# Optimization experiments

Measured on AMD Instinct MI355X. Metric: run time of the kernel, lower is better.

Reference implementation:

```python
import jax, jax.numpy as jnp
import numpy as np

B, N, C, L = 32, 1024, 128, 4

def setup_inputs() -> dict:
    key = jax.random.key(0)
    ks = jax.random.split(key, 8)
    x = jax.random.normal(ks[0], (B, N, C), dtype=jnp.float32)
    # binary adjacency: nonzero entries become unit-weight edges (edge weights unused in module)
    adj = jax.random.randint(ks[1], (B, N, N), 0, 2).astype(jnp.float32)
    mask = jnp.ones((B, N), dtype=jnp.float32)
    s = 1.0 / np.sqrt(C)
    weight = jax.random.uniform(ks[2], (L, C, C), minval=-s, maxval=s, dtype=jnp.float32)
    w_ih = jax.random.uniform(ks[3], (L, 3 * C, C), minval=-s, maxval=s, dtype=jnp.float32)
    w_hh = jax.random.uniform(ks[4], (L, 3 * C, C), minval=-s, maxval=s, dtype=jnp.float32)
    b_ih = jax.random.uniform(ks[5], (L, 3 * C), minval=-s, maxval=s, dtype=jnp.float32)
    b_hh = jax.random.uniform(ks[6], (L, 3 * C), minval=-s, maxval=s, dtype=jnp.float32)
    return {"x": x, "adj": adj, "mask": mask, "weight": weight,
            "w_ih": w_ih, "w_hh": w_hh, "b_ih": b_ih, "b_hh": b_hh}

def _gru_cell(m, h, w_ih, w_hh, b_ih, b_hh):
    # PyTorch GRUCell, gate order (r, z, n)
    gx = m @ w_ih.T + b_ih
    gh = h @ w_hh.T + b_hh
    xr, xz, xn = jnp.split(gx, 3, axis=-1)
    hr, hz, hn = jnp.split(gh, 3, axis=-1)
    r = jax.nn.sigmoid(xr + hr)
    z = jax.nn.sigmoid(xz + hz)
    n = jnp.tanh(xn + r * hn)
    return (1.0 - z) * n + z * h

def reference(x, adj, mask, weight, w_ih, w_hh, b_ih, b_hh):
    h = x  # [B, N, C]; in_channels == out_channels so no zero-padding needed
    for i in range(L):
        hw = jnp.einsum('bnc,cd->bnd', h, weight[i])
        # scatter-add of messages source->target == A^T @ (h W), unit edge weights
        m = jnp.einsum('bjn,bjd->bnd', adj, hw)
        h = _gru_cell(m, h, w_ih[i], w_hh[i], b_ih[i], b_hh[i])
    return h * mask[:, :, None]
```

## Files before the change

### kernel.cpp

```cpp
#include <hip/hip_runtime.h>
#include <stdint.h>


#define NB 32
#define NN 1024
#define NC 128
#define NL 4
#define MTOT (NB * NN)

#define KT 64
#define PITCH 72

typedef __attribute__((ext_vector_type(8))) short s16x8;
typedef __attribute__((ext_vector_type(4))) float f32x4;
typedef __attribute__((ext_vector_type(2))) unsigned int u32x2;
typedef unsigned short U16;
typedef unsigned int U32;

__device__ __forceinline__ U16 f2bf(float f) {
    union { float f; U32 u; } v; v.f = f;
    return (U16)((v.u + 0x7FFFu + ((v.u >> 16) & 1u)) >> 16);
}
__device__ __forceinline__ float bf2f(U16 h) {
    union { U32 u; float f; } v; v.u = ((U32)h) << 16;
    return v.f;
}
__device__ __forceinline__ void splitbf(float x, U16& hi, U16& lo) {
    hi = f2bf(x);
    lo = f2bf(x - bf2f(hi));
}
__device__ __forceinline__ float sigmoidf_(float x) { return 1.f / (1.f + __expf(-x)); }

__device__ __forceinline__ void glds16(const void* g, void* l) {
    __builtin_amdgcn_global_load_lds(
        (const __attribute__((address_space(1))) void*)g,
        (__attribute__((address_space(3))) void*)l, 16, 0, 0);
}

__global__ __launch_bounds__(256) void k_setup(
    const float* __restrict__ adj, U16* __restrict__ adjT,
    const float* __restrict__ w, const float* __restrict__ wih, const float* __restrict__ whh,
    U16* __restrict__ wThi, U16* __restrict__ wTlo,
    U16* __restrict__ wihhi, U16* __restrict__ wihlo,
    U16* __restrict__ whhhi, U16* __restrict__ whhlo,
    const float* __restrict__ x, U16* __restrict__ hhi, U16* __restrict__ hlo)
{
    __shared__ float t[64 * 65];
    const int bid = blockIdx.x, tid = threadIdx.x;
    if (bid < 8192) {
        const int b = bid >> 8, rem = bid & 255;
        const int j0 = (rem & 15) * 64, n0 = (rem >> 4) * 64;
        const int rr = tid >> 4, c4 = (tid & 15) * 4;
#pragma unroll
        for (int p = 0; p < 4; ++p) {
            int j = p * 16 + rr;
            f32x4 v = *(const f32x4*)&adj[((size_t)b << 20) + ((size_t)(j0 + j) << 10) + n0 + c4];
#pragma unroll
            for (int u = 0; u < 4; ++u) t[j * 65 + c4 + u] = v[u];
        }
        __syncthreads();
#pragma unroll
        for (int p = 0; p < 4; ++p) {
            int n = p * 16 + rr;
            U16 h0 = f2bf(t[(c4 + 0) * 65 + n]);
            U16 h1 = f2bf(t[(c4 + 1) * 65 + n]);
            U16 h2 = f2bf(t[(c4 + 2) * 65 + n]);
            U16 h3 = f2bf(t[(c4 + 3) * 65 + n]);
            u32x2 pk; pk[0] = (U32)h0 | ((U32)h1 << 16); pk[1] = (U32)h2 | ((U32)h3 << 16);
            *(u32x2*)&adjT[((size_t)b << 20) + ((size_t)(n0 + n) << 10) + j0 + c4] = pk;
        }
    } else if (bid < 9984) {
        int i = (bid - 8192) * 256 + tid;
        if (i < 65536) {
            int l = i >> 14, rem = i & 16383, c = rem >> 7, d = rem & 127;
            U16 hi, lo; splitbf(w[i], hi, lo);
            int o = (l << 14) + (d << 7) + c;
            wThi[o] = hi; wTlo[o] = lo;
        } else if (i < 262144) {
            int j = i - 65536;
            U16 hi, lo; splitbf(wih[j], hi, lo);
            wihhi[j] = hi; wihlo[j] = lo;
        } else {
            int j = i - 262144;
            U16 hi, lo; splitbf(whh[j], hi, lo);
            whhhi[j] = hi; whhlo[j] = lo;
        }
    } else {
        int base = (bid - 9984) * 2048 + tid;
#pragma unroll
        for (int p = 0; p < 8; ++p) {
            int i = base + p * 256;
            U16 hi, lo; splitbf(x[i], hi, lo);
            hhi[i] = hi; hlo[i] = lo;
        }
    }
}

struct __align__(16) Smem3 {
    union {
        struct { U16 A[2][128 * PITCH]; U16 B[2][128 * PITCH]; } s;
        float bounce[128 * 129];
    };
};

__global__ __launch_bounds__(256, 2) void k_hw(
    const U16* __restrict__ Ahi, const U16* __restrict__ Alo,
    const U16* __restrict__ Bhi, const U16* __restrict__ Blo,
    U16* __restrict__ Ohi, U16* __restrict__ Olo)
{
    __shared__ Smem3 sm;
    const int tid = threadIdx.x;
    const int lane = tid & 63, wv = tid >> 6;
    const int wr = (wv & 1) * 64, wc = (wv >> 1) * 64;
    const int lm = lane & 15, lk8 = (lane >> 4) * 8;
    const int m0 = blockIdx.x * 128;

    f32x4 acc[4][4] = {};

    for (int kc = 0; kc < 128; kc += KT) {
#pragma unroll
        for (int t = 0; t < 4; ++t) {
            int i = tid + t * 256; int r = i >> 3, v = (i & 7) * 8;
            *(s16x8*)&sm.s.A[0][r * PITCH + v] = *(const s16x8*)&Ahi[(size_t)(m0 + r) * 128 + kc + v];
            *(s16x8*)&sm.s.A[1][r * PITCH + v] = *(const s16x8*)&Alo[(size_t)(m0 + r) * 128 + kc + v];
        }
#pragma unroll
        for (int t = 0; t < 4; ++t) {
            int i = tid + t * 256; int r = i >> 3, v = (i & 7) * 8;
            *(s16x8*)&sm.s.B[0][r * PITCH + v] = *(const s16x8*)&Bhi[r * 128 + kc + v];
            *(s16x8*)&sm.s.B[1][r * PITCH + v] = *(const s16x8*)&Blo[r * 128 + kc + v];
        }
        __syncthreads();
#pragma unroll
        for (int ks = 0; ks < 2; ++ks) {
            const int ko = ks * 32 + lk8;
            s16x8 ahi[4], alo[4], bhi[4], blo[4];
#pragma unroll
            for (int q = 0; q < 4; ++q) {
                ahi[q] = *(const s16x8*)&sm.s.A[0][(wr + q * 16 + lm) * PITCH + ko];
                alo[q] = *(const s16x8*)&sm.s.A[1][(wr + q * 16 + lm) * PITCH + ko];
                bhi[q] = *(const s16x8*)&sm.s.B[0][(wc + q * 16 + lm) * PITCH + ko];
                blo[q] = *(const s16x8*)&sm.s.B[1][(wc + q * 16 + lm) * PITCH + ko];
            }
#pragma unroll
            for (int rt = 0; rt < 4; ++rt)
#pragma unroll
                for (int ct = 0; ct < 4; ++ct) {
                    f32x4 a = acc[rt][ct];
                    a = __builtin_amdgcn_mfma_f32_16x16x32_bf16(ahi[rt], bhi[ct], a, 0, 0, 0);
                    a = __builtin_amdgcn_mfma_f32_16x16x32_bf16(ahi[rt], blo[ct], a, 0, 0, 0);
                    a = __builtin_amdgcn_mfma_f32_16x16x32_bf16(alo[rt], bhi[ct], a, 0, 0, 0);
                    acc[rt][ct] = a;
                }
        }
        __syncthreads();
    }
#pragma unroll
    for (int rt = 0; rt < 4; ++rt)
#pragma unroll
        for (int ct = 0; ct < 4; ++ct)
#pragma unroll
            for (int r = 0; r < 4; ++r)
                sm.bounce[(wr + rt * 16 + (lane >> 4) * 4 + r) * 129 + wc + ct * 16 + lm] = acc[rt][ct][r];
    __syncthreads();
    const int b = m0 >> 10, j0 = m0 & 1023;
    for (int t = 0; t < 32; ++t) {
        int i = tid + t * 256; int d = i >> 6, j2 = (i & 63) * 2;
        float x0 = sm.bounce[j2 * 129 + d], x1 = sm.bounce[(j2 + 1) * 129 + d];
        U16 h0, l0, h1, l1; splitbf(x0, h0, l0); splitbf(x1, h1, l1);
        size_t o = (((size_t)(b * 128 + d)) << 10) + j0 + j2;
        *(U32*)&Ohi[o] = (U32)h0 | ((U32)h1 << 16);
        *(U32*)&Olo[o] = (U32)l0 | ((U32)l1 << 16);
    }
}

__global__ __launch_bounds__(256, 2) void k_mega2(
    const U16* __restrict__ adjT,
    const U16* __restrict__ hwThi, const U16* __restrict__ hwTlo,
    U16* mhi, U16* mlo,
    const U16* __restrict__ hhi, const U16* __restrict__ hlo,
    const U16* __restrict__ wihhi, const U16* __restrict__ wihlo,
    const U16* __restrict__ whhhi, const U16* __restrict__ whhlo,
    const float* __restrict__ bih, const float* __restrict__ bhh,
    const float* __restrict__ mask,
    U16* __restrict__ houthi, U16* __restrict__ houtlo,
    float* __restrict__ out, int last)
{
    __shared__ U16 As[64 * 64];
    __shared__ U16 Bh[128 * 64];
    __shared__ U16 Bl[128 * 64];
    const int tid = threadIdx.x;
    const int lane = tid & 63, wv = tid >> 6;
    const int wd0 = wv * 32;
    const int lm = lane & 15, lk8 = (lane >> 4) * 8, quad = lane >> 4;
    const int bt = blockIdx.x >> 4;
    const int n0 = (blockIdx.x & 15) * 64;
    const int row0 = bt * NN + n0;

    f32x4 macc[4][2] = {};
    for (int kc = 0; kc < NN; kc += 64) {
#pragma unroll
        for (int t = 0; t < 2; ++t) {
            int li = tid + t * 256; int r = li >> 3, sg = li & 7;
            glds16(&adjT[((size_t)bt << 20) + ((size_t)(n0 + r) << 10) + kc + sg * 8],
                   &As[li * 8]);
        }
#pragma unroll
        for (int t = 0; t < 4; ++t) {
            int li = tid + t * 256; int d = li >> 3, sg = li & 7;
            size_t o = (((size_t)(bt * 128 + d)) << 10) + kc + sg * 8;
            glds16(&hwThi[o], &Bh[li * 8]);
            glds16(&hwTlo[o], &Bl[li * 8]);
        }
        __syncthreads();
#pragma unroll
        for (int ks = 0; ks < 2; ++ks) {
            const int ko = ks * 32 + lk8;
            s16x8 a[4], bh[2], bl[2];
#pragma unroll
            for (int q = 0; q < 4; ++q)
                a[q] = *(const s16x8*)&As[(q * 16 + lm) * 64 + ko];
#pragma unroll
            for (int q = 0; q < 2; ++q) {
                bh[q] = *(const s16x8*)&Bh[(wd0 + q * 16 + lm) * 64 + ko];
                bl[q] = *(const s16x8*)&Bl[(wd0 + q * 16 + lm) * 64 + ko];
            }
#pragma unroll
            for (int rt = 0; rt < 4; ++rt)
#pragma unroll
                for (int ct = 0; ct < 2; ++ct) {
                    f32x4 c = macc[rt][ct];
                    c = __builtin_amdgcn_mfma_f32_16x16x32_bf16(a[rt], bh[ct], c, 0, 0, 0);
                    c = __builtin_amdgcn_mfma_f32_16x16x32_bf16(a[rt], bl[ct], c, 0, 0, 0);
                    macc[rt][ct] = c;
                }
        }
        __syncthreads();
    }

#pragma unroll
    for (int rt = 0; rt < 4; ++rt)
#pragma unroll
        for (int ct = 0; ct < 2; ++ct)
#pragma unroll
            for (int rr = 0; rr < 4; ++rr) {
                int rloc = rt * 16 + quad * 4 + rr;
                int d = wd0 + ct * 16 + lm;
                U16 hi, lo; splitbf(macc[rt][ct][rr], hi, lo);
                size_t o = (size_t)(row0 + rloc) * 128 + d;
                mhi[o] = hi; mlo[o] = lo;
            }
    __syncthreads();

    f32x4 aR[4][2], aZ[4][2], aXN[4][2], aHN[4][2];
#pragma unroll
    for (int ct = 0; ct < 2; ++ct) {
        const int col = wd0 + ct * 16 + lm;
        const float bR  = bih[col]       + bhh[col];
        const float bZ  = bih[128 + col] + bhh[128 + col];
        const float bXN = bih[256 + col];
        const float bHN = bhh[256 + col];
#pragma unroll
        for (int rt = 0; rt < 4; ++rt) {
            aR[rt][ct]  = f32x4{bR, bR, bR, bR};
            aZ[rt][ct]  = f32x4{bZ, bZ, bZ, bZ};
            aXN[rt][ct] = f32x4{bXN, bXN, bXN, bXN};
            aHN[rt][ct] = f32x4{bHN, bHN, bHN, bHN};
        }
    }

    for (int ch = 0; ch < 4; ++ch) {
        const U16* Ahi = (ch < 2) ? (const U16*)mhi : hhi;
        const U16* Alo = (ch < 2) ? (const U16*)mlo : hlo;
        const U16* __restrict__ Whi = (ch < 2) ? wihhi : whhhi;
        const U16* __restrict__ Wlo = (ch < 2) ? wihlo : whhlo;
        const int kb = (ch & 1) * 64;
#pragma unroll
        for (int ks = 0; ks < 2; ++ks) {
            const int ko = kb + ks * 32 + lk8;
            s16x8 ahi[4], alo[4];
#pragma unroll
            for (int q = 0; q < 4; ++q) {
                size_t ao = (size_t)(row0 + q * 16 + lm) * 128 + ko;
                ahi[q] = *(const s16x8*)&Ahi[ao];
                alo[q] = *(const s16x8*)&Alo[ao];
            }
#pragma unroll
            for (int ct = 0; ct < 2; ++ct) {
                const int col = wd0 + ct * 16 + lm;
                s16x8 bhiR = *(const s16x8*)&Whi[(size_t)col * 128 + ko];
                s16x8 bloR = *(const s16x8*)&Wlo[(size_t)col * 128 + ko];
                s16x8 bhiZ = *(const s16x8*)&Whi[(size_t)(128 + col) * 128 + ko];
                s16x8 bloZ = *(const s16x8*)&Wlo[(size_t)(128 + col) * 128 + ko];
                s16x8 bhiN = *(const s16x8*)&Whi[(size_t)(256 + col) * 128 + ko];
                s16x8 bloN = *(const s16x8*)&Wlo[(size_t)(256 + col) * 128 + ko];
#pragma unroll
                for (int rt = 0; rt < 4; ++rt) {
                    f32x4 r = aR[rt][ct];
                    r = __builtin_amdgcn_mfma_f32_16x16x32_bf16(ahi[rt], bhiR, r, 0, 0, 0);
                    r = __builtin_amdgcn_mfma_f32_16x16x32_bf16(ahi[rt], bloR, r, 0, 0, 0);
                    r = __builtin_amdgcn_mfma_f32_16x16x32_bf16(alo[rt], bhiR, r, 0, 0, 0);
                    aR[rt][ct] = r;
                    f32x4 z = aZ[rt][ct];
                    z = __builtin_amdgcn_mfma_f32_16x16x32_bf16(ahi[rt], bhiZ, z, 0, 0, 0);
                    z = __builtin_amdgcn_mfma_f32_16x16x32_bf16(ahi[rt], bloZ, z, 0, 0, 0);
                    z = __builtin_amdgcn_mfma_f32_16x16x32_bf16(alo[rt], bhiZ, z, 0, 0, 0);
                    aZ[rt][ct] = z;
                }
                if (ch < 2) {
#pragma unroll
                    for (int rt = 0; rt < 4; ++rt) {
                        f32x4 n = aXN[rt][ct];
                        n = __builtin_amdgcn_mfma_f32_16x16x32_bf16(ahi[rt], bhiN, n, 0, 0, 0);
                        n = __builtin_amdgcn_mfma_f32_16x16x32_bf16(ahi[rt], bloN, n, 0, 0, 0);
                        n = __builtin_amdgcn_mfma_f32_16x16x32_bf16(alo[rt], bhiN, n, 0, 0, 0);
                        aXN[rt][ct] = n;
                    }
                } else {
#pragma unroll
                    for (int rt = 0; rt < 4; ++rt) {
                        f32x4 n = aHN[rt][ct];
                        n = __builtin_amdgcn_mfma_f32_16x16x32_bf16(ahi[rt], bhiN, n, 0, 0, 0);
                        n = __builtin_amdgcn_mfma_f32_16x16x32_bf16(ahi[rt], bloN, n, 0, 0, 0);
                        n = __builtin_amdgcn_mfma_f32_16x16x32_bf16(alo[rt], bhiN, n, 0, 0, 0);
                        aHN[rt][ct] = n;
                    }
                }
            }
        }
    }

#pragma unroll
    for (int rt = 0; rt < 4; ++rt) {
#pragma unroll
        for (int ct = 0; ct < 2; ++ct) {
            const int col = wd0 + ct * 16 + lm;
#pragma unroll
            for (int rr = 0; rr < 4; ++rr) {
                const int row = row0 + rt * 16 + quad * 4 + rr;
                float r = sigmoidf_(aR[rt][ct][rr]);
                float z = sigmoidf_(aZ[rt][ct][rr]);
                float n = tanhf(aXN[rt][ct][rr] + r * aHN[rt][ct][rr]);
                size_t ho = (size_t)row * 128 + col;
                float hv = bf2f(hhi[ho]) + bf2f(hlo[ho]);
                float hnew = (1.f - z) * n + z * hv;
                if (last) {
                    out[ho] = hnew * mask[row];
                } else {
                    U16 hi2, lo2; splitbf(hnew, hi2, lo2);
                    houthi[ho] = hi2;
                    houtlo[ho] = lo2;
                }
            }
        }
    }
}

extern "C" void kernel_launch(void* const* d_in, const int* in_sizes, int n_in,
                              void* d_out, int out_size, void* d_ws, size_t ws_size,
                              hipStream_t stream) {
    (void)in_sizes; (void)n_in; (void)out_size; (void)ws_size;
    const float* x    = (const float*)d_in[0];
    const float* adj  = (const float*)d_in[1];
    const float* mask = (const float*)d_in[2];
    const float* wgt  = (const float*)d_in[3];
    const float* wih  = (const float*)d_in[4];
    const float* whh  = (const float*)d_in[5];
    const float* bih  = (const float*)d_in[6];
    const float* bhh  = (const float*)d_in[7];
    float* out = (float*)d_out;

    char* p = (char*)d_ws;
    U16* adjT    = (U16*)p;                p += (size_t)NB * NN * NN * 2;
    U16* h_hi    = (U16*)p;                p += (size_t)MTOT * NC * 2;
    U16* h_lo    = (U16*)p;                p += (size_t)MTOT * NC * 2;
    U16* hwT_hi  = (U16*)p;                p += (size_t)NB * NC * NN * 2;
    U16* hwT_lo  = (U16*)p;                p += (size_t)NB * NC * NN * 2;
    U16* m_hi    = (U16*)p;                p += (size_t)MTOT * NC * 2;
    U16* m_lo    = (U16*)p;                p += (size_t)MTOT * NC * 2;
    U16* wT_hi   = (U16*)p;                p += (size_t)NL * NC * NC * 2;
    U16* wT_lo   = (U16*)p;                p += (size_t)NL * NC * NC * 2;
    U16* wih_hi  = (U16*)p;                p += (size_t)NL * 384 * NC * 2;
    U16* wih_lo  = (U16*)p;                p += (size_t)NL * 384 * NC * 2;
    U16* whh_hi  = (U16*)p;                p += (size_t)NL * 384 * NC * 2;
    U16* whh_lo  = (U16*)p;                p += (size_t)NL * 384 * NC * 2;

    k_setup<<<12032, 256, 0, stream>>>(adj, adjT, wgt, wih, whh,
                                       wT_hi, wT_lo, wih_hi, wih_lo, whh_hi, whh_lo,
                                       x, h_hi, h_lo);

    for (int l = 0; l < NL; ++l) {
        k_hw<<<256, 256, 0, stream>>>(h_hi, h_lo,
                                      wT_hi + l * 16384, wT_lo + l * 16384,
                                      hwT_hi, hwT_lo);
        k_mega2<<<512, 256, 0, stream>>>(adjT, hwT_hi, hwT_lo, m_hi, m_lo, h_hi, h_lo,
                                         wih_hi + l * 49152, wih_lo + l * 49152,
                                         whh_hi + l * 49152, whh_lo + l * 49152,
                                         bih + l * 384, bhh + l * 384, mask,
                                         h_hi, h_lo, out, (l == NL - 1) ? 1 : 0);
    }
}
```

Measured before the change: 606.9 us.

## Double-buffer LDS tiles in the aggregation GEMM and remap blocks per XCD

The adjacency-times-hw K loop now uses two LDS buffers. The next 64-wide K chunk is loaded asynchronously while MFMAs run on the current one, and there is one barrier per iteration instead of two. Block indices are also remapped so that the 64 blocks working on four consecutive batches are spread across the 8 XCDs by the low index bits, meant to keep each batch's hwT slice in one XCD's L2. The cost is twice the LDS footprint (about 80KB per block), which could limit occupancy at two blocks per CU.

Result: no change. 609.7 us (+0.5%).

```diff
diff --git a/kernel.cpp b/kernel.cpp
--- a/kernel.cpp
+++ b/kernel.cpp
@@ -174,7 +174,7 @@
     }
 }
 
-__global__ __launch_bounds__(256, 2) void k_mega2(
+__global__ __launch_bounds__(256, 2) void k_mega3(
     const U16* __restrict__ adjT,
     const U16* __restrict__ hwThi, const U16* __restrict__ hwTlo,
     U16* mhi, U16* mlo,
@@ -186,57 +186,66 @@
     U16* __restrict__ houthi, U16* __restrict__ houtlo,
     float* __restrict__ out, int last)
 {
-    __shared__ U16 As[64 * 64];
-    __shared__ U16 Bh[128 * 64];
-    __shared__ U16 Bl[128 * 64];
+    __shared__ U16 As[2][64 * 64];
+    __shared__ U16 Bh[2][128 * 64];
+    __shared__ U16 Bl[2][128 * 64];
     const int tid = threadIdx.x;
     const int lane = tid & 63, wv = tid >> 6;
     const int wd0 = wv * 32;
     const int lm = lane & 15, lk8 = (lane >> 4) * 8, quad = lane >> 4;
-    const int bt = blockIdx.x >> 4;
-    const int n0 = (blockIdx.x & 15) * 64;
+    const int xcd = blockIdx.x & 7;
+    const int j = blockIdx.x >> 3;
+    const int bt = xcd * 4 + (j >> 4);
+    const int n0 = (j & 15) * 64;
     const int row0 = bt * NN + n0;
 
+#define STAGE(kc, b)                                                                   \
+    {                                                                                  \
+        _Pragma("unroll")                                                              \
+        for (int t = 0; t < 2; ++t) {                                                  \
+            int li = tid + t * 256; int r = li >> 3, sg = li & 7;                      \
+            glds16(&adjT[((size_t)bt << 20) + ((size_t)(n0 + r) << 10) + (kc) + sg * 8], \
+                   &As[b][li * 8]);                                                    \
+        }                                                                              \
+        _Pragma("unroll")                                                              \
+        for (int t = 0; t < 4; ++t) {                                                  \
+            int li = tid + t * 256; int d = li >> 3, sg = li & 7;                      \
+            size_t o = (((size_t)(bt * 128 + d)) << 10) + (kc) + sg * 8;               \
+            glds16(&hwThi[o], &Bh[b][li * 8]);                                         \
+            glds16(&hwTlo[o], &Bl[b][li * 8]);                                         \
+        }                                                                              \
+    }
+
     f32x4 macc[4][2] = {};
-    for (int kc = 0; kc < NN; kc += 64) {
-#pragma unroll
-        for (int t = 0; t < 2; ++t) {
-            int li = tid + t * 256; int r = li >> 3, sg = li & 7;
-            glds16(&adjT[((size_t)bt << 20) + ((size_t)(n0 + r) << 10) + kc + sg * 8],
-                   &As[li * 8]);
-        }
-#pragma unroll
-        for (int t = 0; t < 4; ++t) {
-            int li = tid + t * 256; int d = li >> 3, sg = li & 7;
-            size_t o = (((size_t)(bt * 128 + d)) << 10) + kc + sg * 8;
-            glds16(&hwThi[o], &Bh[li * 8]);
-            glds16(&hwTlo[o], &Bl[li * 8]);
-        }
+    STAGE(0, 0);
+    for (int c = 0; c < 16; ++c) {
+        const int b = c & 1;
         __syncthreads();
+        if (c + 1 < 16) STAGE((c + 1) * 64, b ^ 1);
 #pragma unroll
         for (int ks = 0; ks < 2; ++ks) {
             const int ko = ks * 32 + lk8;
             s16x8 a[4], bh[2], bl[2];
 #pragma unroll
             for (int q = 0; q < 4; ++q)
-                a[q] = *(const s16x8*)&As[(q * 16 + lm) * 64 + ko];
+                a[q] = *(const s16x8*)&As[b][(q * 16 + lm) * 64 + ko];
 #pragma unroll
             for (int q = 0; q < 2; ++q) {
-                bh[q] = *(const s16x8*)&Bh[(wd0 + q * 16 + lm) * 64 + ko];
-                bl[q] = *(const s16x8*)&Bl[(wd0 + q * 16 + lm) * 64 + ko];
+                bh[q] = *(const s16x8*)&Bh[b][(wd0 + q * 16 + lm) * 64 + ko];
+                bl[q] = *(const s16x8*)&Bl[b][(wd0 + q * 16 + lm) * 64 + ko];
             }
 #pragma unroll
             for (int rt = 0; rt < 4; ++rt)
 #pragma unroll
                 for (int ct = 0; ct < 2; ++ct) {
-                    f32x4 c = macc[rt][ct];
-                    c = __builtin_amdgcn_mfma_f32_16x16x32_bf16(a[rt], bh[ct], c, 0, 0, 0);
-                    c = __builtin_amdgcn_mfma_f32_16x16x32_bf16(a[rt], bl[ct], c, 0, 0, 0);
-                    macc[rt][ct] = c;
+                    f32x4 cc = macc[rt][ct];
+                    cc = __builtin_amdgcn_mfma_f32_16x16x32_bf16(a[rt], bh[ct], cc, 0, 0, 0);
+                    cc = __builtin_amdgcn_mfma_f32_16x16x32_bf16(a[rt], bl[ct], cc, 0, 0, 0);
+                    macc[rt][ct] = cc;
                 }
         }
-        __syncthreads();
-    }
+    }
+#undef STAGE
 
 #pragma unroll
     for (int rt = 0; rt < 4; ++rt)
@@ -393,7 +402,7 @@
         k_hw<<<256, 256, 0, stream>>>(h_hi, h_lo,
                                       wT_hi + l * 16384, wT_lo + l * 16384,
                                       hwT_hi, hwT_lo);
-        k_mega2<<<512, 256, 0, stream>>>(adjT, hwT_hi, hwT_lo, m_hi, m_lo, h_hi, h_lo,
+        k_mega3<<<512, 256, 0, stream>>>(adjT, hwT_hi, hwT_lo, m_hi, m_lo, h_hi, h_lo,
                                          wih_hi + l * 49152, wih_lo + l * 49152,
                                          whh_hi + l * 49152, whh_lo + l * 49152,
                                          bih + l * 384, bhh + l * 384, mask,
```
